# Optimization experiments

Hardware: AMD Instinct MI355X
Metric: run time of the kernel (lower is better)

The kernel has to match this reference:

```python
import jax, jax.numpy as jnp
import numpy as np

STRIDE = 1
PAD = 1
K = 3  # kernel size


def setup_inputs() -> dict:
    key = jax.random.key(0)
    k1, k2, k3, k4 = jax.random.split(key, 4)
    B, C, H, W, O = 4, 256, 64, 64, 256
    x = jax.random.normal(k1, (B, C, H, W), jnp.float32)
    offset = jax.random.normal(k2, (B, 2 * K * K, H, W), jnp.float32)
    mask = jax.random.uniform(k3, (B, K * K, H, W), jnp.float32)
    # kaiming-ish scale for the conv weight
    weight = jax.random.normal(k4, (O, C, K, K), jnp.float32) / np.float32(np.sqrt(C * K * K))
    return {"x": x, "offset": offset, "mask": mask, "weight": weight}


def _deform_conv2d(x, offset, mask, weight, stride=STRIDE, pad=PAD):
    """Modulated deformable conv v2 (torchvision deform_conv2d semantics)."""
    B, C, H, W = x.shape
    O, _, Kh, Kw = weight.shape
    KK = Kh * Kw
    Ho = (H + 2 * pad - Kh) // stride + 1
    Wo = (W + 2 * pad - Kw) // stride + 1

    # offset layout: [B, 2*KK, Ho, Wo], pairs are (dy, dx) per kernel tap
    off = offset.reshape(B, KK, 2, Ho, Wo)
    dy, dx = off[:, :, 0], off[:, :, 1]  # [B, KK, Ho, Wo]

    ki = (jnp.arange(KK) // Kw).astype(x.dtype)  # kernel row per tap
    kj = (jnp.arange(KK) % Kw).astype(x.dtype)   # kernel col per tap
    base_y = (jnp.arange(Ho) * stride - pad).astype(x.dtype)
    base_x = (jnp.arange(Wo) * stride - pad).astype(x.dtype)

    # sampling positions [B, KK, Ho, Wo]
    py = base_y[None, None, :, None] + ki[None, :, None, None] + dy
    px = base_x[None, None, None, :] + kj[None, :, None, None] + dx

    y0 = jnp.floor(py)
    x0 = jnp.floor(px)
    wy = py - y0  # fractional weights
    wx = px - x0
    y0i = y0.astype(jnp.int32)
    x0i = x0.astype(jnp.int32)

    x_bhwc = jnp.transpose(x, (0, 2, 3, 1))  # [B, H, W, C] for gathers
    b_idx = jnp.arange(B)[:, None, None, None]

    def gather(yi, xi):
        # zero outside the image (zero-padding bilinear sampling)
        valid = (yi >= 0) & (yi < H) & (xi >= 0) & (xi < W)
        v = x_bhwc[b_idx, jnp.clip(yi, 0, H - 1), jnp.clip(xi, 0, W - 1)]  # [B,KK,Ho,Wo,C]
        return v * valid[..., None].astype(x.dtype)

    one = jnp.asarray(1, x.dtype)
    sampled = (gather(y0i, x0i) * ((one - wy) * (one - wx))[..., None]
               + gather(y0i, x0i + 1) * ((one - wy) * wx)[..., None]
               + gather(y0i + 1, x0i) * (wy * (one - wx))[..., None]
               + gather(y0i + 1, x0i + 1) * (wy * wx)[..., None])

    sampled = sampled * mask.reshape(B, KK, Ho, Wo)[..., None]  # modulation

    # weighted accumulation == implicit GEMM over (c, kk)
    return jnp.einsum('bkhwc,ock->bohw', sampled, weight.reshape(O, C, KK))


def reference(x, offset, mask, weight):
    return _deform_conv2d(x, offset, mask, weight)
```

## Files before the change

kernel.cpp:

```cpp
#include <hip/hip_runtime.h>
#include <hip/hip_bf16.h>

#define BN 4
#define CN 256
#define HN 64
#define WN 64
#define ON 256
#define KKN 9
#define HWN 4096
#define KDIM 2304
#define KC 288

using frag_ab = __attribute__((ext_vector_type(8))) short;
using frag_cd = __attribute__((ext_vector_type(4))) float;
using short4v = __attribute__((ext_vector_type(4))) short;

static __device__ inline short f2bf(float f) {
    union { float f; unsigned u; } v; v.f = f;
    unsigned r = v.u + 0x7fffu + ((v.u >> 16) & 1u);
    return (short)(r >> 16);
}
static __device__ inline float bf2f(short s) {
    union { unsigned u; float f; } v; v.u = ((unsigned)(unsigned short)s) << 16;
    return v.f;
}

__global__ __launch_bounds__(256) void prep_kernel(const float* __restrict__ x,
                                                   const float* __restrict__ wsrc,
                                                   short* __restrict__ xb16,
                                                   short* __restrict__ wtb) {
    int bidx = blockIdx.x;
    int tid  = threadIdx.x;
    if (bidx < 1024) {
        __shared__ float tile[64][65];
        int b   = bidx >> 8;
        int rem = bidx & 255;
        int c0  = (rem >> 6) * 64;
        int p0  = (rem & 63) * 64;
        int tp = tid & 63, tc = tid >> 6;
        for (int i = 0; i < 16; ++i) {
            int c = tc + i * 4;
            tile[c][tp] = x[(b * CN + c0 + c) * HWN + p0 + tp];
        }
        __syncthreads();
        int tcc = tid & 63, tpp = tid >> 6;
        for (int i = 0; i < 16; ++i) {
            int p = tpp + i * 4;
            xb16[(b * HWN + p0 + p) * CN + c0 + tcc] = f2bf(tile[tcc][p]);
        }
    } else {
        int chunk = (bidx - 1024) * 256 + tid;
        int ob  = chunk / (KC * 64);
        int rem = chunk - ob * (KC * 64);
        int kc  = rem >> 6;
        int row = rem & 63;
        int o   = ob * 64 + row;
        int kk  = kc >> 5;
        int oct = kc & 31;
        frag_ab v;
        #pragma unroll
        for (int e = 0; e < 8; ++e)
            v[e] = f2bf(wsrc[(o * CN + oct * 8 + e) * 9 + kk]);
        *(frag_ab*)&wtb[(size_t)chunk * 8] = v;
    }
}

__global__ __launch_bounds__(256, 2) void fused_kernel(const short* __restrict__ xb16,
                                                       const short* __restrict__ wtb,
                                                       const float* __restrict__ offs,
                                                       const float* __restrict__ maskp,
                                                       float* __restrict__ out) {
    __shared__ union {
        short Ab[2][8448];
        float outb[32 * 257];
    } sm;
    int tid = threadIdx.x;
    int m0  = blockIdx.x * 32;
    int b   = m0 >> 12;
    int h   = (m0 >> 6) & 63;
    int w0  = m0 & 63;
    int wv  = tid >> 6, lane = tid & 63;
    int q   = lane >> 4, r = lane & 15;
    int wbase = 33 * (lane >> 1) * 8 + (lane & 1) * 4;

    frag_cd acc[2][4];
    #pragma unroll
    for (int i = 0; i < 2; ++i)
        #pragma unroll
        for (int j = 0; j < 4; ++j)
            acc[i][j] = (frag_cd){0.f, 0.f, 0.f, 0.f};

    for (int kk = 0; kk < KKN; ++kk) {
        short* dst = sm.Ab[kk & 1];
        int ki = kk / 3, kj = kk - ki * 3;
        #pragma unroll
        for (int i = 0; i < 8; ++i) {
            int mloc = wv * 8 + i;
            int wc   = w0 + mloc;
            int obase = ((b * 18 + kk * 2) * 64 + h) * 64 + wc;
            float dy = offs[obase];
            float dx = offs[obase + HWN];
            float mv = maskp[((b * 9 + kk) * 64 + h) * 64 + wc];
            float py = (float)(h - 1 + ki) + dy;
            float px = (float)(wc - 1 + kj) + dx;
            float y0f = floorf(py), x0f = floorf(px);
            float wy = py - y0f, wx = px - x0f;
            int y0 = (int)y0f, x0 = (int)x0f;
            int   cb[4];
            float cw[4];
            #pragma unroll
            for (int cy = 0; cy < 2; ++cy)
                #pragma unroll
                for (int cx = 0; cx < 2; ++cx) {
                    int yy = y0 + cy, xx = x0 + cx;
                    bool valid = (yy >= 0 && yy < HN && xx >= 0 && xx < WN);
                    int yc = min(max(yy, 0), HN - 1);
                    int xc = min(max(xx, 0), WN - 1);
                    cb[cy * 2 + cx] = ((b * HN + yc) * WN + xc) * CN;
                    float wgt = (cy ? wy : 1.f - wy) * (cx ? wx : 1.f - wx) * mv;
                    cw[cy * 2 + cx] = valid ? wgt : 0.f;
                }
            short4v v[4];
            #pragma unroll
            for (int c = 0; c < 4; ++c)
                v[c] = *(const short4v*)&xb16[cb[c] + lane * 4];
            short4v res;
            #pragma unroll
            for (int e = 0; e < 4; e += 2) {
                float a0 = cw[0] * bf2f(v[0][e]) + cw[1] * bf2f(v[1][e])
                         + cw[2] * bf2f(v[2][e]) + cw[3] * bf2f(v[3][e]);
                float a1 = cw[0] * bf2f(v[0][e + 1]) + cw[1] * bf2f(v[1][e + 1])
                         + cw[2] * bf2f(v[2][e + 1]) + cw[3] * bf2f(v[3][e + 1]);
                __hip_bfloat162 p2 = __float22bfloat162_rn(make_float2(a0, a1));
                res[e]     = *(short*)&p2.x;
                res[e + 1] = *(short*)&p2.y;
            }
            *(short4v*)&dst[wbase + mloc * 8] = res;
        }
        __syncthreads();
        #pragma unroll
        for (int ks = 0; ks < 8; ++ks) {
            frag_ab af[2], bf[4];
            #pragma unroll
            for (int i = 0; i < 2; ++i)
                af[i] = *(const frag_ab*)
                    &dst[(33 * (ks * 4 + q) + i * 16 + r) * 8];
            #pragma unroll
            for (int j = 0; j < 4; ++j)
                bf[j] = *(const frag_ab*)
                    &wtb[(((size_t)wv * KC + kk * 32 + ks * 4 + q) * 64
                          + j * 16 + r) * 8];
            #pragma unroll
            for (int i = 0; i < 2; ++i)
                #pragma unroll
                for (int j = 0; j < 4; ++j)
                    acc[i][j] = __builtin_amdgcn_mfma_f32_16x16x32_bf16(
                        af[i], bf[j], acc[i][j], 0, 0, 0);
        }
    }
    __syncthreads();

    #pragma unroll
    for (int i = 0; i < 2; ++i)
        #pragma unroll
        for (int j = 0; j < 4; ++j) {
            int ml = i * 16 + q * 4;
            int ol = wv * 64 + j * 16 + r;
            sm.outb[(ml + 0) * 257 + ol] = acc[i][j][0];
            sm.outb[(ml + 1) * 257 + ol] = acc[i][j][1];
            sm.outb[(ml + 2) * 257 + ol] = acc[i][j][2];
            sm.outb[(ml + 3) * 257 + ol] = acc[i][j][3];
        }
    __syncthreads();
    {
        int ww = tid & 31;
        int og = tid >> 5;
        #pragma unroll
        for (int oo = 0; oo < 32; ++oo) {
            int o = oo * 8 + og;
            out[(((size_t)b * ON + o) * HN + h) * WN + w0 + ww] =
                sm.outb[ww * 257 + o];
        }
    }
}

extern "C" void kernel_launch(void* const* d_in, const int* in_sizes, int n_in,
                              void* d_out, int out_size, void* d_ws, size_t ws_size,
                              hipStream_t stream) {
    const float* x      = (const float*)d_in[0];
    const float* offset = (const float*)d_in[1];
    const float* mask   = (const float*)d_in[2];
    const float* weight = (const float*)d_in[3];
    float* out = (float*)d_out;

    short* xb16 = (short*)d_ws;
    short* wtb  = (short*)((char*)d_ws + 8388608);

    hipLaunchKernelGGL(prep_kernel,  dim3(1312), dim3(256), 0, stream,
                       x, weight, xb16, wtb);
    hipLaunchKernelGGL(fused_kernel, dim3(512),  dim3(256), 0, stream,
                       xb16, wtb, offset, mask, out);
}
```

Before: 138.1 us.

## Software-pipeline bilinear gathers with MFMA via register prefetch of next tap

```diff
diff --git a/kernel.cpp b/kernel.cpp
--- a/kernel.cpp
+++ b/kernel.cpp
@@ -14,15 +14,19 @@
 using frag_ab = __attribute__((ext_vector_type(8))) short;
 using frag_cd = __attribute__((ext_vector_type(4))) float;
 using short4v = __attribute__((ext_vector_type(4))) short;
+using f32x2   = __attribute__((ext_vector_type(2))) float;
+using f32x4   = __attribute__((ext_vector_type(4))) float;
 
 static __device__ inline short f2bf(float f) {
     union { float f; unsigned u; } v; v.f = f;
     unsigned r = v.u + 0x7fffu + ((v.u >> 16) & 1u);
     return (short)(r >> 16);
 }
-static __device__ inline float bf2f(short s) {
-    union { unsigned u; float f; } v; v.u = ((unsigned)(unsigned short)s) << 16;
-    return v.f;
+static __device__ inline f32x2 unpk(unsigned u) {
+    union { unsigned v; float f; } a, b;
+    a.v = u << 16;
+    b.v = u & 0xffff0000u;
+    f32x2 r; r[0] = a.f; r[1] = b.f; return r;
 }
 
 __global__ __launch_bounds__(256) void prep_kernel(const float* __restrict__ x,
@@ -81,6 +85,7 @@
     int w0  = m0 & 63;
     int wv  = tid >> 6, lane = tid & 63;
     int q   = lane >> 4, r = lane & 15;
+    int wrow0 = w0 + wv * 8;
     int wbase = 33 * (lane >> 1) * 8 + (lane & 1) * 4;
 
     frag_cd acc[2][4];
@@ -90,61 +95,100 @@
         for (int j = 0; j < 4; ++j)
             acc[i][j] = (frag_cd){0.f, 0.f, 0.f, 0.f};
 
+    f32x4   dyS[2][2], dxS[2][2], mvS[2][2];
+    short4v pv[8][4];
+    float   cwv[8][4];
+
+#define LOAD_OFFS(kk, st)                                                   \
+    {                                                                       \
+        int ob_ = ((b * 18 + (kk) * 2) * 64 + h) * 64 + wrow0;              \
+        dyS[st][0] = *(const f32x4*)&offs[ob_];                             \
+        dyS[st][1] = *(const f32x4*)&offs[ob_ + 4];                         \
+        dxS[st][0] = *(const f32x4*)&offs[ob_ + HWN];                       \
+        dxS[st][1] = *(const f32x4*)&offs[ob_ + HWN + 4];                   \
+        int mb_ = ((b * 9 + (kk)) * 64 + h) * 64 + wrow0;                   \
+        mvS[st][0] = *(const f32x4*)&maskp[mb_];                            \
+        mvS[st][1] = *(const f32x4*)&maskp[mb_ + 4];                        \
+    }
+
+#define GATHERS(kk, st)                                                     \
+    {                                                                       \
+        const int ki_ = (kk) / 3, kj_ = (kk) % 3;                           \
+        _Pragma("unroll")                                                   \
+        for (int i = 0; i < 8; ++i) {                                       \
+            float dyi = dyS[st][i >> 2][i & 3];                             \
+            float dxi = dxS[st][i >> 2][i & 3];                             \
+            float mvi = mvS[st][i >> 2][i & 3];                             \
+            int wc = wrow0 + i;                                             \
+            float py = (float)(h - 1 + ki_) + dyi;                          \
+            float px = (float)(wc - 1 + kj_) + dxi;                         \
+            float y0f = floorf(py), x0f = floorf(px);                       \
+            float wy = py - y0f, wx = px - x0f;                             \
+            int y0 = (int)y0f, x0 = (int)x0f;                               \
+            _Pragma("unroll")                                               \
+            for (int cy = 0; cy < 2; ++cy) {                                \
+                _Pragma("unroll")                                           \
+                for (int cx = 0; cx < 2; ++cx) {                            \
+                    int yy = y0 + cy, xx = x0 + cx;                         \
+                    bool valid =                                            \
+                        (yy >= 0 && yy < HN && xx >= 0 && xx < WN);         \
+                    int yc = min(max(yy, 0), HN - 1);                       \
+                    int xc = min(max(xx, 0), WN - 1);                       \
+                    int cb_ = ((b * HN + yc) * WN + xc) * CN;               \
+                    float wgt = (cy ? wy : 1.f - wy) *                      \
+                                (cx ? wx : 1.f - wx) * mvi;                 \
+                    cwv[i][cy * 2 + cx] = valid ? wgt : 0.f;                \
+                    pv[i][cy * 2 + cx] =                                    \
+                        *(const short4v*)&xb16[cb_ + lane * 4];             \
+                }                                                           \
+            }                                                               \
+        }                                                                   \
+    }
+
+#define COMBINE(dstp)                                                       \
+    {                                                                       \
+        short* dst_ = (dstp);                                               \
+        _Pragma("unroll")                                                   \
+        for (int i = 0; i < 8; ++i) {                                       \
+            union { short4v s; unsigned u[2]; } a0, a1, a2, a3;             \
+            a0.s = pv[i][0]; a1.s = pv[i][1];                               \
+            a2.s = pv[i][2]; a3.s = pv[i][3];                               \
+            short4v res;                                                    \
+            _Pragma("unroll")                                               \
+            for (int p = 0; p < 2; ++p) {                                   \
+                f32x2 s2 = unpk(a0.u[p]) * cwv[i][0];                       \
+                s2 += unpk(a1.u[p]) * cwv[i][1];                            \
+                s2 += unpk(a2.u[p]) * cwv[i][2];                            \
+                s2 += unpk(a3.u[p]) * cwv[i][3];                            \
+                __hip_bfloat162 p2 =                                        \
+                    __float22bfloat162_rn(make_float2(s2[0], s2[1]));       \
+                res[2 * p]     = *(short*)&p2.x;                            \
+                res[2 * p + 1] = *(short*)&p2.y;                            \
+            }                                                               \
+            *(short4v*)&dst_[wbase + (wv * 8 + i) * 8] = res;               \
+        }                                                                   \
+    }
+
+    LOAD_OFFS(0, 0)
+    LOAD_OFFS(1, 1)
+    GATHERS(0, 0)
+    COMBINE(sm.Ab[0])
+    __syncthreads();
+
+    #pragma unroll
     for (int kk = 0; kk < KKN; ++kk) {
-        short* dst = sm.Ab[kk & 1];
-        int ki = kk / 3, kj = kk - ki * 3;
-        #pragma unroll
-        for (int i = 0; i < 8; ++i) {
-            int mloc = wv * 8 + i;
-            int wc   = w0 + mloc;
-            int obase = ((b * 18 + kk * 2) * 64 + h) * 64 + wc;
-            float dy = offs[obase];
-            float dx = offs[obase + HWN];
-            float mv = maskp[((b * 9 + kk) * 64 + h) * 64 + wc];
-            float py = (float)(h - 1 + ki) + dy;
-            float px = (float)(wc - 1 + kj) + dx;
-            float y0f = floorf(py), x0f = floorf(px);
-            float wy = py - y0f, wx = px - x0f;
-            int y0 = (int)y0f, x0 = (int)x0f;
-            int   cb[4];
-            float cw[4];
-            #pragma unroll
-            for (int cy = 0; cy < 2; ++cy)
-                #pragma unroll
-                for (int cx = 0; cx < 2; ++cx) {
-                    int yy = y0 + cy, xx = x0 + cx;
-                    bool valid = (yy >= 0 && yy < HN && xx >= 0 && xx < WN);
-                    int yc = min(max(yy, 0), HN - 1);
-                    int xc = min(max(xx, 0), WN - 1);
-                    cb[cy * 2 + cx] = ((b * HN + yc) * WN + xc) * CN;
-                    float wgt = (cy ? wy : 1.f - wy) * (cx ? wx : 1.f - wx) * mv;
-                    cw[cy * 2 + cx] = valid ? wgt : 0.f;
-                }
-            short4v v[4];
-            #pragma unroll
-            for (int c = 0; c < 4; ++c)
-                v[c] = *(const short4v*)&xb16[cb[c] + lane * 4];
-            short4v res;
-            #pragma unroll
-            for (int e = 0; e < 4; e += 2) {
-                float a0 = cw[0] * bf2f(v[0][e]) + cw[1] * bf2f(v[1][e])
-                         + cw[2] * bf2f(v[2][e]) + cw[3] * bf2f(v[3][e]);
-                float a1 = cw[0] * bf2f(v[0][e + 1]) + cw[1] * bf2f(v[1][e + 1])
-                         + cw[2] * bf2f(v[2][e + 1]) + cw[3] * bf2f(v[3][e + 1]);
-                __hip_bfloat162 p2 = __float22bfloat162_rn(make_float2(a0, a1));
-                res[e]     = *(short*)&p2.x;
-                res[e + 1] = *(short*)&p2.y;
-            }
-            *(short4v*)&dst[wbase + mloc * 8] = res;
-        }
-        __syncthreads();
+        short* cur = sm.Ab[kk & 1];
+        if (kk + 1 < KKN) {
+            GATHERS(kk + 1, (kk + 1) & 1)
+            if (kk + 2 < KKN) LOAD_OFFS(kk + 2, kk & 1)
+        }
         #pragma unroll
         for (int ks = 0; ks < 8; ++ks) {
             frag_ab af[2], bf[4];
             #pragma unroll
             for (int i = 0; i < 2; ++i)
                 af[i] = *(const frag_ab*)
-                    &dst[(33 * (ks * 4 + q) + i * 16 + r) * 8];
+                    &cur[(33 * (ks * 4 + q) + i * 16 + r) * 8];
             #pragma unroll
             for (int j = 0; j < 4; ++j)
                 bf[j] = *(const frag_ab*)
@@ -157,8 +201,9 @@
                     acc[i][j] = __builtin_amdgcn_mfma_f32_16x16x32_bf16(
                         af[i], bf[j], acc[i][j], 0, 0, 0);
         }
-    }
-    __syncthreads();
+        if (kk + 1 < KKN) COMBINE(sm.Ab[(kk + 1) & 1])
+        __syncthreads();
+    }
 
     #pragma unroll
     for (int i = 0; i < 2; ++i)
@@ -182,6 +227,9 @@
                 sm.outb[ww * 257 + o];
         }
     }
+#undef LOAD_OFFS
+#undef GATHERS
+#undef COMBINE
 }
 
 extern "C" void kernel_launch(void* const* d_in, const int* in_sizes, int n_in,
```

After: 146.0 us. 1.06x slower.

## Merge prep and fused kernels into one cooperative kernel with grid sync

Applied to the files above, without the earlier changes.

```diff
diff --git a/kernel.cpp b/kernel.cpp
--- a/kernel.cpp
+++ b/kernel.cpp
@@ -1,5 +1,8 @@
 #include <hip/hip_runtime.h>
 #include <hip/hip_bf16.h>
+#include <hip/hip_cooperative_groups.h>
+
+namespace cg = cooperative_groups;
 
 #define BN 4
 #define CN 256
@@ -14,42 +17,62 @@
 using frag_ab = __attribute__((ext_vector_type(8))) short;
 using frag_cd = __attribute__((ext_vector_type(4))) float;
 using short4v = __attribute__((ext_vector_type(4))) short;
+using f32x2   = __attribute__((ext_vector_type(2))) float;
 
 static __device__ inline short f2bf(float f) {
     union { float f; unsigned u; } v; v.f = f;
     unsigned r = v.u + 0x7fffu + ((v.u >> 16) & 1u);
     return (short)(r >> 16);
 }
-static __device__ inline float bf2f(short s) {
-    union { unsigned u; float f; } v; v.u = ((unsigned)(unsigned short)s) << 16;
-    return v.f;
-}
-
-__global__ __launch_bounds__(256) void prep_kernel(const float* __restrict__ x,
-                                                   const float* __restrict__ wsrc,
-                                                   short* __restrict__ xb16,
-                                                   short* __restrict__ wtb) {
-    int bidx = blockIdx.x;
-    int tid  = threadIdx.x;
-    if (bidx < 1024) {
-        __shared__ float tile[64][65];
+static __device__ inline f32x2 unpk(unsigned u) {
+    union { unsigned v; float f; } a, b;
+    a.v = u << 16;
+    b.v = u & 0xffff0000u;
+    f32x2 r; r[0] = a.f; r[1] = b.f; return r;
+}
+static __device__ inline float rlane_f(float v, int l) {
+    union { float f; int i; } u; u.f = v;
+    u.i = __builtin_amdgcn_readlane(u.i, l);
+    return u.f;
+}
+
+__global__ __launch_bounds__(256, 2) void mono_kernel(const float* __restrict__ x,
+                                                      const float* __restrict__ wsrc,
+                                                      const float* __restrict__ offs,
+                                                      const float* __restrict__ maskp,
+                                                      short* __restrict__ xb16,
+                                                      short* __restrict__ wtb,
+                                                      float* __restrict__ out) {
+    __shared__ union {
+        float tile[64][65];
+        short Ab[2][8448];
+        float outb[32 * 257];
+    } sm;
+    int tid = threadIdx.x;
+    int bid = blockIdx.x;
+
+    #pragma unroll 1
+    for (int t = 0; t < 2; ++t) {
+        int bidx = bid * 2 + t;
         int b   = bidx >> 8;
         int rem = bidx & 255;
         int c0  = (rem >> 6) * 64;
         int p0  = (rem & 63) * 64;
         int tp = tid & 63, tc = tid >> 6;
+        __syncthreads();
         for (int i = 0; i < 16; ++i) {
             int c = tc + i * 4;
-            tile[c][tp] = x[(b * CN + c0 + c) * HWN + p0 + tp];
+            sm.tile[c][tp] = x[(b * CN + c0 + c) * HWN + p0 + tp];
         }
         __syncthreads();
         int tcc = tid & 63, tpp = tid >> 6;
         for (int i = 0; i < 16; ++i) {
             int p = tpp + i * 4;
-            xb16[(b * HWN + p0 + p) * CN + c0 + tcc] = f2bf(tile[tcc][p]);
-        }
-    } else {
-        int chunk = (bidx - 1024) * 256 + tid;
+            xb16[(b * HWN + p0 + p) * CN + c0 + tcc] = f2bf(sm.tile[tcc][p]);
+        }
+    }
+    if (tid < 144) {
+        int chunk = bid * 144 + tid;
         int ob  = chunk / (KC * 64);
         int rem = chunk - ob * (KC * 64);
         int kc  = rem >> 6;
@@ -63,25 +86,21 @@
             v[e] = f2bf(wsrc[(o * CN + oct * 8 + e) * 9 + kk]);
         *(frag_ab*)&wtb[(size_t)chunk * 8] = v;
     }
-}
-
-__global__ __launch_bounds__(256, 2) void fused_kernel(const short* __restrict__ xb16,
-                                                       const short* __restrict__ wtb,
-                                                       const float* __restrict__ offs,
-                                                       const float* __restrict__ maskp,
-                                                       float* __restrict__ out) {
-    __shared__ union {
-        short Ab[2][8448];
-        float outb[32 * 257];
-    } sm;
-    int tid = threadIdx.x;
-    int m0  = blockIdx.x * 32;
+    __threadfence();
+    cg::this_grid().sync();
+
+    int m0  = bid * 32;
     int b   = m0 >> 12;
     int h   = (m0 >> 6) & 63;
     int w0  = m0 & 63;
     int wv  = tid >> 6, lane = tid & 63;
     int q   = lane >> 4, r = lane & 15;
+    int wrow0 = w0 + wv * 8;
     int wbase = 33 * (lane >> 1) * 8 + (lane & 1) * 4;
+    int i_  = (lane >> 2) & 7;
+    int cy_ = (lane >> 1) & 1;
+    int cx_ = lane & 1;
+    int wc_ = wrow0 + i_;
 
     frag_cd acc[2][4];
     #pragma unroll
@@ -90,52 +109,54 @@
         for (int j = 0; j < 4; ++j)
             acc[i][j] = (frag_cd){0.f, 0.f, 0.f, 0.f};
 
+    #pragma unroll 1
     for (int kk = 0; kk < KKN; ++kk) {
         short* dst = sm.Ab[kk & 1];
         int ki = kk / 3, kj = kk - ki * 3;
+        float dy = offs[((b * 18 + kk * 2) * 64 + h) * 64 + wc_];
+        float dx = offs[((b * 18 + kk * 2 + 1) * 64 + h) * 64 + wc_];
+        float mv = maskp[((b * 9 + kk) * 64 + h) * 64 + wc_];
+        float py = (float)(h - 1 + ki) + dy;
+        float px = (float)(wc_ - 1 + kj) + dx;
+        float y0f = floorf(py), x0f = floorf(px);
+        float wy = py - y0f, wx = px - x0f;
+        int yy = (int)y0f + cy_;
+        int xx = (int)x0f + cx_;
+        bool valid = (yy >= 0 && yy < HN && xx >= 0 && xx < WN);
+        int yc = min(max(yy, 0), HN - 1);
+        int xc = min(max(xx, 0), WN - 1);
+        int addr = ((b * HN + yc) * WN + xc) * CN;
+        float wgt = (cy_ ? wy : 1.f - wy) * (cx_ ? wx : 1.f - wx) * mv;
+        wgt = valid ? wgt : 0.f;
         #pragma unroll
         for (int i = 0; i < 8; ++i) {
-            int mloc = wv * 8 + i;
-            int wc   = w0 + mloc;
-            int obase = ((b * 18 + kk * 2) * 64 + h) * 64 + wc;
-            float dy = offs[obase];
-            float dx = offs[obase + HWN];
-            float mv = maskp[((b * 9 + kk) * 64 + h) * 64 + wc];
-            float py = (float)(h - 1 + ki) + dy;
-            float px = (float)(wc - 1 + kj) + dx;
-            float y0f = floorf(py), x0f = floorf(px);
-            float wy = py - y0f, wx = px - x0f;
-            int y0 = (int)y0f, x0 = (int)x0f;
-            int   cb[4];
-            float cw[4];
-            #pragma unroll
-            for (int cy = 0; cy < 2; ++cy)
-                #pragma unroll
-                for (int cx = 0; cx < 2; ++cx) {
-                    int yy = y0 + cy, xx = x0 + cx;
-                    bool valid = (yy >= 0 && yy < HN && xx >= 0 && xx < WN);
-                    int yc = min(max(yy, 0), HN - 1);
-                    int xc = min(max(xx, 0), WN - 1);
-                    cb[cy * 2 + cx] = ((b * HN + yc) * WN + xc) * CN;
-                    float wgt = (cy ? wy : 1.f - wy) * (cx ? wx : 1.f - wx) * mv;
-                    cw[cy * 2 + cx] = valid ? wgt : 0.f;
-                }
-            short4v v[4];
-            #pragma unroll
-            for (int c = 0; c < 4; ++c)
-                v[c] = *(const short4v*)&xb16[cb[c] + lane * 4];
+            int   a0 = __builtin_amdgcn_readlane(addr, i * 4 + 0);
+            int   a1 = __builtin_amdgcn_readlane(addr, i * 4 + 1);
+            int   a2 = __builtin_amdgcn_readlane(addr, i * 4 + 2);
+            int   a3 = __builtin_amdgcn_readlane(addr, i * 4 + 3);
+            float w0s = rlane_f(wgt, i * 4 + 0);
+            float w1s = rlane_f(wgt, i * 4 + 1);
+            float w2s = rlane_f(wgt, i * 4 + 2);
+            float w3s = rlane_f(wgt, i * 4 + 3);
+            short4v v0 = *(const short4v*)&xb16[a0 + lane * 4];
+            short4v v1 = *(const short4v*)&xb16[a1 + lane * 4];
+            short4v v2 = *(const short4v*)&xb16[a2 + lane * 4];
+            short4v v3 = *(const short4v*)&xb16[a3 + lane * 4];
+            union { short4v s; unsigned u[2]; } u0, u1, u2, u3;
+            u0.s = v0; u1.s = v1; u2.s = v2; u3.s = v3;
             short4v res;
             #pragma unroll
-            for (int e = 0; e < 4; e += 2) {
-                float a0 = cw[0] * bf2f(v[0][e]) + cw[1] * bf2f(v[1][e])
-                         + cw[2] * bf2f(v[2][e]) + cw[3] * bf2f(v[3][e]);
-                float a1 = cw[0] * bf2f(v[0][e + 1]) + cw[1] * bf2f(v[1][e + 1])
-                         + cw[2] * bf2f(v[2][e + 1]) + cw[3] * bf2f(v[3][e + 1]);
-                __hip_bfloat162 p2 = __float22bfloat162_rn(make_float2(a0, a1));
-                res[e]     = *(short*)&p2.x;
-                res[e + 1] = *(short*)&p2.y;
+            for (int p = 0; p < 2; ++p) {
+                f32x2 s2 = unpk(u0.u[p]) * w0s;
+                s2 += unpk(u1.u[p]) * w1s;
+                s2 += unpk(u2.u[p]) * w2s;
+                s2 += unpk(u3.u[p]) * w3s;
+                __hip_bfloat162 p2 =
+                    __float22bfloat162_rn(make_float2(s2[0], s2[1]));
+                res[2 * p]     = *(short*)&p2.x;
+                res[2 * p + 1] = *(short*)&p2.y;
             }
-            *(short4v*)&dst[wbase + mloc * 8] = res;
+            *(short4v*)&dst[wbase + (wv * 8 + i) * 8] = res;
         }
         __syncthreads();
         #pragma unroll
@@ -196,8 +217,8 @@
     short* xb16 = (short*)d_ws;
     short* wtb  = (short*)((char*)d_ws + 8388608);
 
-    hipLaunchKernelGGL(prep_kernel,  dim3(1312), dim3(256), 0, stream,
-                       x, weight, xb16, wtb);
-    hipLaunchKernelGGL(fused_kernel, dim3(512),  dim3(256), 0, stream,
-                       xb16, wtb, offset, mask, out);
-}
+    void* args[] = { (void*)&x, (void*)&weight, (void*)&offset, (void*)&mask,
+                     (void*)&xb16, (void*)&wtb, (void*)&out };
+    hipLaunchCooperativeKernel((const void*)mono_kernel, dim3(512), dim3(256),
+                               args, 0, stream);
+}
```

New measurement: 279.9 us. 2.03x slower.
